# Performance work log

Measured on AMD Instinct MI355X. Metric: run time of the kernel, lower is better.

## Reference

```python
import jax, jax.numpy as jnp
import numpy as np

NH = 16

def sinusoidal_pos(pos, nh=NH):
    # pos: [B, L] -> P: [B, L, nh], interleaved sin/cos with integer multiples of pi
    freqs = jnp.arange(1, nh // 2 + 1, dtype=pos.dtype) * jnp.pi  # [nh/2]
    ang = pos[..., None] * freqs                                   # [B, L, nh/2]
    # interleave: even channels sin, odd channels cos
    P = jnp.stack([jnp.sin(ang), jnp.cos(ang)], axis=-1)           # [B, L, nh/2, 2]
    return P.reshape(*pos.shape, nh)


def setup_inputs() -> dict:
    key = jax.random.key(0)
    k1, k2, k3, k4, k5, k6 = jax.random.split(key, 6)
    B, L, nx, nh = 2048, 1024, 8, NH
    return {
        "x": jax.random.normal(k1, (B, L, nx), dtype=jnp.float32),
        "pos": jax.random.uniform(k2, (B, L), dtype=jnp.float32),
        "W_q": jax.random.normal(k3, (nh, nx), dtype=jnp.float32) * 0.1,
        "W_k": jax.random.normal(k4, (nh, nx), dtype=jnp.float32) * 0.1,
        "W_v": jax.random.normal(k5, (nh, nx), dtype=jnp.float32) * 0.1,
        "W_o": jax.random.normal(k6, (nh, nh), dtype=jnp.float32) * 0.1,
    }


def reference(x, pos, W_q, W_k, W_v, W_o):
    # x: [B, L, nx]; pos: [B, L]; Linear weights are [out, in] (torch convention)
    q = jnp.einsum("blx,hx->blh", x, W_q)
    k = jnp.einsum("blx,hx->blh", x, W_k)
    v = jnp.einsum("blx,hx->blh", x, W_v)
    P = sinusoidal_pos(pos, W_q.shape[0])
    q = q + P
    k = k + P
    L = q.shape[1]
    # channel-wise attention: score over feature dim, [B, nh, nh]
    score = jnp.einsum("bld,ble->bde", q, k) / jnp.sqrt(jnp.asarray(L, q.dtype))
    attn = jax.nn.softmax(score, axis=-1)
    out = jnp.einsum("bde,ble->bdl", attn, v)   # [B, nh, L]
    out = jnp.einsum("bdl,hd->blh", out, W_o)   # transpose then W_o: [B, L, nh]
    return out
```

## Files before the change

kernel.cpp:

```cpp
#include <hip/hip_runtime.h>
#include <cstdint>
#include <cstddef>

#define LSEQ 1024
#define NH   16
#define NX   8

__device__ __forceinline__ uint32_t f2bf(float f) {
    uint32_t u = __float_as_uint(f);
    u += 0x7fffu + ((u >> 16) & 1u);
    return u >> 16;
}
__device__ __forceinline__ float bflo(uint32_t w) { return __uint_as_float(w << 16); }
__device__ __forceinline__ float bfhi(uint32_t w) { return __uint_as_float(w & 0xffff0000u); }

__global__ __launch_bounds__(256, 1)
void attn_fused_kernel(const float* __restrict__ x, const float* __restrict__ pos,
                       const float* __restrict__ Wq, const float* __restrict__ Wk,
                       const float* __restrict__ Wv, const float* __restrict__ Wo,
                       float* __restrict__ out) {
    __shared__ __align__(16) char smem_raw[65536];
    uint16_t* q_lds = (uint16_t*)smem_raw;
    uint16_t* k_lds = (uint16_t*)(smem_raw + 32768);
    float* scorebuf = (float*)smem_raw;
    float* attn_s   = (float*)(smem_raw + 4096);
    float* M_s      = (float*)(smem_raw + 5120);
    float* weff_s   = (float*)(smem_raw + 6144);

    const int tid = threadIdx.x;
    const int b   = blockIdx.x;
    const float* xb = x   + (size_t)b * LSEQ * NX;
    const float* pb = pos + (size_t)b * LSEQ;

    {
        const int dg   = tid >> 6;
        const int lidx = tid & 63;
        float wq[4][8], wk[4][8];
        #pragma unroll
        for (int r = 0; r < 4; ++r) {
            const float4 a0 = *(const float4*)(Wq + (4 * dg + r) * 8);
            const float4 a1 = *(const float4*)(Wq + (4 * dg + r) * 8 + 4);
            const float4 b0 = *(const float4*)(Wk + (4 * dg + r) * 8);
            const float4 b1 = *(const float4*)(Wk + (4 * dg + r) * 8 + 4);
            wq[r][0]=a0.x; wq[r][1]=a0.y; wq[r][2]=a0.z; wq[r][3]=a0.w;
            wq[r][4]=a1.x; wq[r][5]=a1.y; wq[r][6]=a1.z; wq[r][7]=a1.w;
            wk[r][0]=b0.x; wk[r][1]=b0.y; wk[r][2]=b0.z; wk[r][3]=b0.w;
            wk[r][4]=b1.x; wk[r][5]=b1.y; wk[r][6]=b1.z; wk[r][7]=b1.w;
        }
        const float f0 = (float)(2 * dg + 1);
        const float f1 = (float)(2 * dg + 2);
        for (int p = 0; p < 16; ++p) {
            const int l = p * 64 + lidx;
            const float4 xa = *(const float4*)(xb + (size_t)l * 8);
            const float4 xc = *(const float4*)(xb + (size_t)l * 8 + 4);
            const float pv = pb[l];
            float pe[4];
            pe[0] = sinpif(pv * f0); pe[1] = cospif(pv * f0);
            pe[2] = sinpif(pv * f1); pe[3] = cospif(pv * f1);
            float qv[4], kv[4];
            #pragma unroll
            for (int r = 0; r < 4; ++r) {
                qv[r] = xa.x*wq[r][0] + xa.y*wq[r][1] + xa.z*wq[r][2] + xa.w*wq[r][3]
                      + xc.x*wq[r][4] + xc.y*wq[r][5] + xc.z*wq[r][6] + xc.w*wq[r][7] + pe[r];
                kv[r] = xa.x*wk[r][0] + xa.y*wk[r][1] + xa.z*wk[r][2] + xa.w*wk[r][3]
                      + xc.x*wk[r][4] + xc.y*wk[r][5] + xc.z*wk[r][6] + xc.w*wk[r][7] + pe[r];
            }
            uint2 qp, kp;
            qp.x = f2bf(qv[0]) | (f2bf(qv[1]) << 16);
            qp.y = f2bf(qv[2]) | (f2bf(qv[3]) << 16);
            kp.x = f2bf(kv[0]) | (f2bf(kv[1]) << 16);
            kp.y = f2bf(kv[2]) | (f2bf(kv[3]) << 16);
            *(uint2*)(q_lds + (size_t)l * 16 + 4 * dg) = qp;
            *(uint2*)(k_lds + (size_t)l * 16 + 4 * dg) = kp;
        }
    }
    __syncthreads();

    {
        const int lg = tid >> 4;
        const int dt = (tid >> 2) & 3;
        const int et = tid & 3;
        float acc[4][4];
        #pragma unroll
        for (int i = 0; i < 4; ++i)
            #pragma unroll
            for (int j = 0; j < 4; ++j) acc[i][j] = 0.f;

        const uint16_t* qp = q_lds + lg * 16 + dt * 4;
        const uint16_t* kp = k_lds + lg * 16 + et * 4;
        #pragma unroll 4
        for (int i = 0; i < 64; ++i) {
            const uint2 qw = *(const uint2*)(qp + i * 256);
            const uint2 kw = *(const uint2*)(kp + i * 256);
            const float q0 = bflo(qw.x), q1 = bfhi(qw.x), q2 = bflo(qw.y), q3 = bfhi(qw.y);
            const float k0 = bflo(kw.x), k1 = bfhi(kw.x), k2 = bflo(kw.y), k3 = bfhi(kw.y);
            acc[0][0] += q0*k0; acc[0][1] += q0*k1; acc[0][2] += q0*k2; acc[0][3] += q0*k3;
            acc[1][0] += q1*k0; acc[1][1] += q1*k1; acc[1][2] += q1*k2; acc[1][3] += q1*k3;
            acc[2][0] += q2*k0; acc[2][1] += q2*k1; acc[2][2] += q2*k2; acc[2][3] += q2*k3;
            acc[3][0] += q3*k0; acc[3][1] += q3*k1; acc[3][2] += q3*k2; acc[3][3] += q3*k3;
        }
        #pragma unroll
        for (int di = 0; di < 4; ++di)
            #pragma unroll
            for (int ei = 0; ei < 4; ++ei) {
                acc[di][ei] += __shfl_xor(acc[di][ei], 16);
                acc[di][ei] += __shfl_xor(acc[di][ei], 32);
            }
        __syncthreads();
        const int lane = tid & 63;
        const int w    = tid >> 6;
        if (lane < 16) {
            #pragma unroll
            for (int di = 0; di < 4; ++di)
                #pragma unroll
                for (int ei = 0; ei < 4; ++ei)
                    scorebuf[w * 256 + (dt * 4 + di) * 16 + (et * 4 + ei)] = acc[di][ei];
        }
    }
    __syncthreads();

    {
        const int e = tid & 15;
        float s = scorebuf[tid] + scorebuf[256 + tid] + scorebuf[512 + tid] + scorebuf[768 + tid];
        s *= 0.03125f;
        float mx = s;
        #pragma unroll
        for (int m = 1; m < 16; m <<= 1) mx = fmaxf(mx, __shfl_xor(mx, m));
        const float ex = __expf(s - mx);
        float sum = ex;
        #pragma unroll
        for (int m = 1; m < 16; m <<= 1) sum += __shfl_xor(sum, m);
        attn_s[tid] = ex / sum;
        __syncthreads();

        const int h = tid >> 4;
        float acc = 0.f;
        #pragma unroll
        for (int d = 0; d < 16; ++d) acc += Wo[h * 16 + d] * attn_s[d * 16 + e];
        M_s[h * 16 + e] = acc;
        __syncthreads();

        if (tid < 128) {
            const int hh = tid >> 3, xc = tid & 7;
            float wv = 0.f;
            #pragma unroll
            for (int ee = 0; ee < 16; ++ee) wv += M_s[hh * 16 + ee] * Wv[ee * 8 + xc];
            weff_s[hh * 8 + xc] = wv;
        }
    }
    __syncthreads();

    {
        float xr[4][8];
        #pragma unroll
        for (int r = 0; r < 4; ++r) {
            const int l = tid + 256 * r;
            const float4 a = *(const float4*)(xb + (size_t)l * 8);
            const float4 c = *(const float4*)(xb + (size_t)l * 8 + 4);
            xr[r][0]=a.x; xr[r][1]=a.y; xr[r][2]=a.z; xr[r][3]=a.w;
            xr[r][4]=c.x; xr[r][5]=c.y; xr[r][6]=c.z; xr[r][7]=c.w;
        }
        float o[4][16];
        #pragma unroll
        for (int h = 0; h < 16; ++h) {
            const float4 wA = *(const float4*)(weff_s + h * 8);
            const float4 wB = *(const float4*)(weff_s + h * 8 + 4);
            #pragma unroll
            for (int r = 0; r < 4; ++r) {
                o[r][h] = xr[r][0]*wA.x + xr[r][1]*wA.y + xr[r][2]*wA.z + xr[r][3]*wA.w
                        + xr[r][4]*wB.x + xr[r][5]*wB.y + xr[r][6]*wB.z + xr[r][7]*wB.w;
            }
        }
        #pragma unroll
        for (int r = 0; r < 4; ++r) {
            const size_t base = ((size_t)b * LSEQ + tid + 256 * r) * NH;
            #pragma unroll
            for (int g = 0; g < 4; ++g) {
                *(float4*)(out + base + g * 4) =
                    make_float4(o[r][g*4+0], o[r][g*4+1], o[r][g*4+2], o[r][g*4+3]);
            }
        }
    }
}

extern "C" void kernel_launch(void* const* d_in, const int* in_sizes, int n_in,
                              void* d_out, int out_size, void* d_ws, size_t ws_size,
                              hipStream_t stream) {
    const float* x   = (const float*)d_in[0];
    const float* pos = (const float*)d_in[1];
    const float* Wq  = (const float*)d_in[2];
    const float* Wk  = (const float*)d_in[3];
    const float* Wv  = (const float*)d_in[4];
    const float* Wo  = (const float*)d_in[5];
    float* out = (float*)d_out;
    const int B = in_sizes[1] / LSEQ;
    attn_fused_kernel<<<B, 256, 0, stream>>>(x, pos, Wq, Wk, Wv, Wo, out);
}
```

Measured before the change: 97.68 us.

## Split fused attention into chunked score-partial kernel and output kernel

```diff
diff --git a/kernel.cpp b/kernel.cpp
--- a/kernel.cpp
+++ b/kernel.cpp
@@ -2,9 +2,12 @@
 #include <cstdint>
 #include <cstddef>
 
-#define LSEQ 1024
-#define NH   16
-#define NX   8
+#define LSEQ   1024
+#define NH     16
+#define NX     8
+#define CHUNKS 4
+#define ROWS   256
+#define STR    20
 
 __device__ __forceinline__ uint32_t f2bf(float f) {
     uint32_t u = __float_as_uint(f);
@@ -13,6 +16,187 @@
 }
 __device__ __forceinline__ float bflo(uint32_t w) { return __uint_as_float(w << 16); }
 __device__ __forceinline__ float bfhi(uint32_t w) { return __uint_as_float(w & 0xffff0000u); }
+
+__global__ __launch_bounds__(256, 4)
+void score_partial_kernel(const float* __restrict__ x, const float* __restrict__ pos,
+                          const float* __restrict__ Wq, const float* __restrict__ Wk,
+                          float* __restrict__ g_part) {
+    __shared__ __align__(16) uint16_t q_lds[ROWS * STR];
+    __shared__ __align__(16) uint16_t k_lds[ROWS * STR];
+    __shared__ float scorebuf[4 * 256];
+
+    const int tid = threadIdx.x;
+    const int bid = blockIdx.x;
+    const int b   = bid >> 2;
+    const int c   = bid & 3;
+    const float* xb = x   + ((size_t)b * LSEQ + c * ROWS) * NX;
+    const float* pb = pos + (size_t)b * LSEQ + c * ROWS;
+
+    {
+        const int dg   = tid >> 6;
+        const int lidx = tid & 63;
+        float wq[4][8], wk[4][8];
+        #pragma unroll
+        for (int r = 0; r < 4; ++r) {
+            const float4 a0 = *(const float4*)(Wq + (4 * dg + r) * 8);
+            const float4 a1 = *(const float4*)(Wq + (4 * dg + r) * 8 + 4);
+            const float4 b0 = *(const float4*)(Wk + (4 * dg + r) * 8);
+            const float4 b1 = *(const float4*)(Wk + (4 * dg + r) * 8 + 4);
+            wq[r][0]=a0.x; wq[r][1]=a0.y; wq[r][2]=a0.z; wq[r][3]=a0.w;
+            wq[r][4]=a1.x; wq[r][5]=a1.y; wq[r][6]=a1.z; wq[r][7]=a1.w;
+            wk[r][0]=b0.x; wk[r][1]=b0.y; wk[r][2]=b0.z; wk[r][3]=b0.w;
+            wk[r][4]=b1.x; wk[r][5]=b1.y; wk[r][6]=b1.z; wk[r][7]=b1.w;
+        }
+        const float f0 = (float)(2 * dg + 1);
+        const float f1 = (float)(2 * dg + 2);
+        #pragma unroll
+        for (int p = 0; p < ROWS / 64; ++p) {
+            const int l = p * 64 + lidx;
+            const float4 xa = *(const float4*)(xb + (size_t)l * 8);
+            const float4 xc = *(const float4*)(xb + (size_t)l * 8 + 4);
+            const float pv = pb[l];
+            float pe[4];
+            pe[0] = sinpif(pv * f0); pe[1] = cospif(pv * f0);
+            pe[2] = sinpif(pv * f1); pe[3] = cospif(pv * f1);
+            float qv[4], kv[4];
+            #pragma unroll
+            for (int r = 0; r < 4; ++r) {
+                qv[r] = xa.x*wq[r][0] + xa.y*wq[r][1] + xa.z*wq[r][2] + xa.w*wq[r][3]
+                      + xc.x*wq[r][4] + xc.y*wq[r][5] + xc.z*wq[r][6] + xc.w*wq[r][7] + pe[r];
+                kv[r] = xa.x*wk[r][0] + xa.y*wk[r][1] + xa.z*wk[r][2] + xa.w*wk[r][3]
+                      + xc.x*wk[r][4] + xc.y*wk[r][5] + xc.z*wk[r][6] + xc.w*wk[r][7] + pe[r];
+            }
+            uint2 qp, kp;
+            qp.x = f2bf(qv[0]) | (f2bf(qv[1]) << 16);
+            qp.y = f2bf(qv[2]) | (f2bf(qv[3]) << 16);
+            kp.x = f2bf(kv[0]) | (f2bf(kv[1]) << 16);
+            kp.y = f2bf(kv[2]) | (f2bf(kv[3]) << 16);
+            *(uint2*)(q_lds + (size_t)l * STR + 4 * dg) = qp;
+            *(uint2*)(k_lds + (size_t)l * STR + 4 * dg) = kp;
+        }
+    }
+    __syncthreads();
+
+    {
+        const int lg = tid >> 4;
+        const int dt = (tid >> 2) & 3;
+        const int et = tid & 3;
+        float acc[4][4];
+        #pragma unroll
+        for (int i = 0; i < 4; ++i)
+            #pragma unroll
+            for (int j = 0; j < 4; ++j) acc[i][j] = 0.f;
+
+        const uint16_t* qp = q_lds + lg * STR + dt * 4;
+        const uint16_t* kp = k_lds + lg * STR + et * 4;
+        #pragma unroll 4
+        for (int i = 0; i < ROWS / 16; ++i) {
+            const uint2 qw = *(const uint2*)(qp + i * 16 * STR);
+            const uint2 kw = *(const uint2*)(kp + i * 16 * STR);
+            const float q0 = bflo(qw.x), q1 = bfhi(qw.x), q2 = bflo(qw.y), q3 = bfhi(qw.y);
+            const float k0 = bflo(kw.x), k1 = bfhi(kw.x), k2 = bflo(kw.y), k3 = bfhi(kw.y);
+            acc[0][0] += q0*k0; acc[0][1] += q0*k1; acc[0][2] += q0*k2; acc[0][3] += q0*k3;
+            acc[1][0] += q1*k0; acc[1][1] += q1*k1; acc[1][2] += q1*k2; acc[1][3] += q1*k3;
+            acc[2][0] += q2*k0; acc[2][1] += q2*k1; acc[2][2] += q2*k2; acc[2][3] += q2*k3;
+            acc[3][0] += q3*k0; acc[3][1] += q3*k1; acc[3][2] += q3*k2; acc[3][3] += q3*k3;
+        }
+        #pragma unroll
+        for (int di = 0; di < 4; ++di)
+            #pragma unroll
+            for (int ei = 0; ei < 4; ++ei) {
+                acc[di][ei] += __shfl_xor(acc[di][ei], 16);
+                acc[di][ei] += __shfl_xor(acc[di][ei], 32);
+            }
+        const int lane = tid & 63;
+        const int w    = tid >> 6;
+        if (lane < 16) {
+            #pragma unroll
+            for (int di = 0; di < 4; ++di)
+                #pragma unroll
+                for (int ei = 0; ei < 4; ++ei)
+                    scorebuf[w * 256 + (dt * 4 + di) * 16 + (et * 4 + ei)] = acc[di][ei];
+        }
+    }
+    __syncthreads();
+    g_part[(size_t)bid * 256 + tid] =
+        scorebuf[tid] + scorebuf[256 + tid] + scorebuf[512 + tid] + scorebuf[768 + tid];
+}
+
+__global__ __launch_bounds__(256, 4)
+void out_kernel(const float* __restrict__ x, const float* __restrict__ Wv,
+                const float* __restrict__ Wo, const float* __restrict__ g_part,
+                float* __restrict__ out) {
+    __shared__ float attn_s[256];
+    __shared__ float M_s[256];
+    __shared__ float weff_s[128];
+
+    const int tid = threadIdx.x;
+    const int b   = blockIdx.x;
+    const float* xb = x + (size_t)b * LSEQ * NX;
+
+    {
+        const float* gp = g_part + (size_t)(b * CHUNKS) * 256 + tid;
+        float s = gp[0] + gp[256] + gp[512] + gp[768];
+        s *= 0.03125f;
+        float mx = s;
+        #pragma unroll
+        for (int m = 1; m < 16; m <<= 1) mx = fmaxf(mx, __shfl_xor(mx, m));
+        const float ex = __expf(s - mx);
+        float sum = ex;
+        #pragma unroll
+        for (int m = 1; m < 16; m <<= 1) sum += __shfl_xor(sum, m);
+        attn_s[tid] = ex / sum;
+    }
+    __syncthreads();
+    {
+        const int h = tid >> 4, e = tid & 15;
+        float acc = 0.f;
+        #pragma unroll
+        for (int d = 0; d < 16; ++d) acc += Wo[h * 16 + d] * attn_s[d * 16 + e];
+        M_s[h * 16 + e] = acc;
+    }
+    __syncthreads();
+    if (tid < 128) {
+        const int hh = tid >> 3, xc = tid & 7;
+        float wv = 0.f;
+        #pragma unroll
+        for (int ee = 0; ee < 16; ++ee) wv += M_s[hh * 16 + ee] * Wv[ee * 8 + xc];
+        weff_s[hh * 8 + xc] = wv;
+    }
+    __syncthreads();
+
+    {
+        float xr[4][8];
+        #pragma unroll
+        for (int r = 0; r < 4; ++r) {
+            const int l = tid + 256 * r;
+            const float4 a = *(const float4*)(xb + (size_t)l * 8);
+            const float4 c = *(const float4*)(xb + (size_t)l * 8 + 4);
+            xr[r][0]=a.x; xr[r][1]=a.y; xr[r][2]=a.z; xr[r][3]=a.w;
+            xr[r][4]=c.x; xr[r][5]=c.y; xr[r][6]=c.z; xr[r][7]=c.w;
+        }
+        float o[4][16];
+        #pragma unroll
+        for (int h = 0; h < 16; ++h) {
+            const float4 wA = *(const float4*)(weff_s + h * 8);
+            const float4 wB = *(const float4*)(weff_s + h * 8 + 4);
+            #pragma unroll
+            for (int r = 0; r < 4; ++r) {
+                o[r][h] = xr[r][0]*wA.x + xr[r][1]*wA.y + xr[r][2]*wA.z + xr[r][3]*wA.w
+                        + xr[r][4]*wB.x + xr[r][5]*wB.y + xr[r][6]*wB.z + xr[r][7]*wB.w;
+            }
+        }
+        #pragma unroll
+        for (int r = 0; r < 4; ++r) {
+            const size_t base = ((size_t)b * LSEQ + tid + 256 * r) * NH;
+            #pragma unroll
+            for (int g = 0; g < 4; ++g) {
+                *(float4*)(out + base + g * 4) =
+                    make_float4(o[r][g*4+0], o[r][g*4+1], o[r][g*4+2], o[r][g*4+3]);
+            }
+        }
+    }
+}
 
 __global__ __launch_bounds__(256, 1)
 void attn_fused_kernel(const float* __restrict__ x, const float* __restrict__ pos,
@@ -75,7 +259,6 @@
         }
     }
     __syncthreads();
-
     {
         const int lg = tid >> 4;
         const int dt = (tid >> 2) & 3;
@@ -85,7 +268,6 @@
         for (int i = 0; i < 4; ++i)
             #pragma unroll
             for (int j = 0; j < 4; ++j) acc[i][j] = 0.f;
-
         const uint16_t* qp = q_lds + lg * 16 + dt * 4;
         const uint16_t* kp = k_lds + lg * 16 + et * 4;
         #pragma unroll 4
@@ -118,9 +300,7 @@
         }
     }
     __syncthreads();
-
-    {
-        const int e = tid & 15;
+    {
         float s = scorebuf[tid] + scorebuf[256 + tid] + scorebuf[512 + tid] + scorebuf[768 + tid];
         s *= 0.03125f;
         float mx = s;
@@ -132,14 +312,12 @@
         for (int m = 1; m < 16; m <<= 1) sum += __shfl_xor(sum, m);
         attn_s[tid] = ex / sum;
         __syncthreads();
-
-        const int h = tid >> 4;
+        const int h = tid >> 4, e = tid & 15;
         float acc = 0.f;
         #pragma unroll
         for (int d = 0; d < 16; ++d) acc += Wo[h * 16 + d] * attn_s[d * 16 + e];
         M_s[h * 16 + e] = acc;
         __syncthreads();
-
         if (tid < 128) {
             const int hh = tid >> 3, xc = tid & 7;
             float wv = 0.f;
@@ -149,7 +327,6 @@
         }
     }
     __syncthreads();
-
     {
         float xr[4][8];
         #pragma unroll
@@ -194,5 +371,13 @@
     const float* Wo  = (const float*)d_in[5];
     float* out = (float*)d_out;
     const int B = in_sizes[1] / LSEQ;
-    attn_fused_kernel<<<B, 256, 0, stream>>>(x, pos, Wq, Wk, Wv, Wo, out);
-}
+
+    const size_t ws_needed = (size_t)B * CHUNKS * 256 * sizeof(float);
+    if (ws_size >= ws_needed) {
+        float* g_part = (float*)d_ws;
+        score_partial_kernel<<<B * CHUNKS, 256, 0, stream>>>(x, pos, Wq, Wk, g_part);
+        out_kernel<<<B, 256, 0, stream>>>(x, Wv, Wo, g_part, out);
+    } else {
+        attn_fused_kernel<<<B, 256, 0, stream>>>(x, pos, Wq, Wk, Wv, Wo, out);
+    }
+}
```

After: 159.1 us. 1.63x slower.

## Use 512-thread blocks with XOR-swizzled LDS layout for Q/K

Applied to the files above, without the earlier changes.

```diff
diff --git a/kernel.cpp b/kernel.cpp
--- a/kernel.cpp
+++ b/kernel.cpp
@@ -14,18 +14,18 @@
 __device__ __forceinline__ float bflo(uint32_t w) { return __uint_as_float(w << 16); }
 __device__ __forceinline__ float bfhi(uint32_t w) { return __uint_as_float(w & 0xffff0000u); }
 
-__global__ __launch_bounds__(256, 1)
-void attn_fused_kernel(const float* __restrict__ x, const float* __restrict__ pos,
-                       const float* __restrict__ Wq, const float* __restrict__ Wk,
-                       const float* __restrict__ Wv, const float* __restrict__ Wo,
-                       float* __restrict__ out) {
+__global__ __launch_bounds__(512, 4)
+void attn_fused512(const float* __restrict__ x, const float* __restrict__ pos,
+                   const float* __restrict__ Wq, const float* __restrict__ Wk,
+                   const float* __restrict__ Wv, const float* __restrict__ Wo,
+                   float* __restrict__ out) {
     __shared__ __align__(16) char smem_raw[65536];
     uint16_t* q_lds = (uint16_t*)smem_raw;
     uint16_t* k_lds = (uint16_t*)(smem_raw + 32768);
     float* scorebuf = (float*)smem_raw;
-    float* attn_s   = (float*)(smem_raw + 4096);
-    float* M_s      = (float*)(smem_raw + 5120);
-    float* weff_s   = (float*)(smem_raw + 6144);
+    float* attn_s   = (float*)(smem_raw + 8192);
+    float* M_s      = (float*)(smem_raw + 9216);
+    float* weff_s   = (float*)(smem_raw + 10240);
 
     const int tid = threadIdx.x;
     const int b   = blockIdx.x;
@@ -33,8 +33,8 @@
     const float* pb = pos + (size_t)b * LSEQ;
 
     {
-        const int dg   = tid >> 6;
-        const int lidx = tid & 63;
+        const int dg   = tid >> 7;
+        const int lidx = tid & 127;
         float wq[4][8], wk[4][8];
         #pragma unroll
         for (int r = 0; r < 4; ++r) {
@@ -49,8 +49,9 @@
         }
         const float f0 = (float)(2 * dg + 1);
         const float f1 = (float)(2 * dg + 2);
-        for (int p = 0; p < 16; ++p) {
-            const int l = p * 64 + lidx;
+        #pragma unroll
+        for (int p = 0; p < 8; ++p) {
+            const int l = p * 128 + lidx;
             const float4 xa = *(const float4*)(xb + (size_t)l * 8);
             const float4 xc = *(const float4*)(xb + (size_t)l * 8 + 4);
             const float pv = pb[l];
@@ -70,28 +71,30 @@
             qp.y = f2bf(qv[2]) | (f2bf(qv[3]) << 16);
             kp.x = f2bf(kv[0]) | (f2bf(kv[1]) << 16);
             kp.y = f2bf(kv[2]) | (f2bf(kv[3]) << 16);
-            *(uint2*)(q_lds + (size_t)l * 16 + 4 * dg) = qp;
-            *(uint2*)(k_lds + (size_t)l * 16 + 4 * dg) = kp;
-        }
-    }
-    __syncthreads();
-
+            const int sw = ((l >> 2) & 3) ^ dg;
+            *(uint2*)(q_lds + (size_t)l * 16 + sw * 4) = qp;
+            *(uint2*)(k_lds + (size_t)l * 16 + sw * 4) = kp;
+        }
+    }
+    __syncthreads();
+
+    float acc[4][4];
     {
         const int lg = tid >> 4;
         const int dt = (tid >> 2) & 3;
         const int et = tid & 3;
-        float acc[4][4];
         #pragma unroll
         for (int i = 0; i < 4; ++i)
             #pragma unroll
             for (int j = 0; j < 4; ++j) acc[i][j] = 0.f;
 
-        const uint16_t* qp = q_lds + lg * 16 + dt * 4;
-        const uint16_t* kp = k_lds + lg * 16 + et * 4;
+        const int s = (lg >> 2) & 3;
+        const uint16_t* qp = q_lds + lg * 16 + (dt ^ s) * 4;
+        const uint16_t* kp = k_lds + lg * 16 + (et ^ s) * 4;
         #pragma unroll 4
-        for (int i = 0; i < 64; ++i) {
-            const uint2 qw = *(const uint2*)(qp + i * 256);
-            const uint2 kw = *(const uint2*)(kp + i * 256);
+        for (int i = 0; i < 32; ++i) {
+            const uint2 qw = *(const uint2*)(qp + i * 512);
+            const uint2 kw = *(const uint2*)(kp + i * 512);
             const float q0 = bflo(qw.x), q1 = bfhi(qw.x), q2 = bflo(qw.y), q3 = bfhi(qw.y);
             const float k0 = bflo(kw.x), k1 = bfhi(kw.x), k2 = bflo(kw.y), k3 = bfhi(kw.y);
             acc[0][0] += q0*k0; acc[0][1] += q0*k1; acc[0][2] += q0*k2; acc[0][3] += q0*k3;
@@ -119,9 +122,10 @@
     }
     __syncthreads();
 
-    {
-        const int e = tid & 15;
-        float s = scorebuf[tid] + scorebuf[256 + tid] + scorebuf[512 + tid] + scorebuf[768 + tid];
+    if (tid < 256) {
+        float s = 0.f;
+        #pragma unroll
+        for (int w = 0; w < 8; ++w) s += scorebuf[w * 256 + tid];
         s *= 0.03125f;
         float mx = s;
         #pragma unroll
@@ -131,49 +135,49 @@
         #pragma unroll
         for (int m = 1; m < 16; m <<= 1) sum += __shfl_xor(sum, m);
         attn_s[tid] = ex / sum;
-        __syncthreads();
-
-        const int h = tid >> 4;
-        float acc = 0.f;
-        #pragma unroll
-        for (int d = 0; d < 16; ++d) acc += Wo[h * 16 + d] * attn_s[d * 16 + e];
-        M_s[h * 16 + e] = acc;
-        __syncthreads();
-
-        if (tid < 128) {
-            const int hh = tid >> 3, xc = tid & 7;
-            float wv = 0.f;
-            #pragma unroll
-            for (int ee = 0; ee < 16; ++ee) wv += M_s[hh * 16 + ee] * Wv[ee * 8 + xc];
-            weff_s[hh * 8 + xc] = wv;
-        }
+    }
+    __syncthreads();
+    if (tid < 256) {
+        const int h = tid >> 4, e = tid & 15;
+        float acc2 = 0.f;
+        #pragma unroll
+        for (int d = 0; d < 16; ++d) acc2 += Wo[h * 16 + d] * attn_s[d * 16 + e];
+        M_s[h * 16 + e] = acc2;
+    }
+    __syncthreads();
+    if (tid < 128) {
+        const int hh = tid >> 3, xc = tid & 7;
+        float wv = 0.f;
+        #pragma unroll
+        for (int ee = 0; ee < 16; ++ee) wv += M_s[hh * 16 + ee] * Wv[ee * 8 + xc];
+        weff_s[hh * 8 + xc] = wv;
     }
     __syncthreads();
 
     {
-        float xr[4][8];
-        #pragma unroll
-        for (int r = 0; r < 4; ++r) {
-            const int l = tid + 256 * r;
+        float xr[2][8];
+        #pragma unroll
+        for (int r = 0; r < 2; ++r) {
+            const int l = tid + 512 * r;
             const float4 a = *(const float4*)(xb + (size_t)l * 8);
             const float4 c = *(const float4*)(xb + (size_t)l * 8 + 4);
             xr[r][0]=a.x; xr[r][1]=a.y; xr[r][2]=a.z; xr[r][3]=a.w;
             xr[r][4]=c.x; xr[r][5]=c.y; xr[r][6]=c.z; xr[r][7]=c.w;
         }
-        float o[4][16];
+        float o[2][16];
         #pragma unroll
         for (int h = 0; h < 16; ++h) {
             const float4 wA = *(const float4*)(weff_s + h * 8);
             const float4 wB = *(const float4*)(weff_s + h * 8 + 4);
             #pragma unroll
-            for (int r = 0; r < 4; ++r) {
+            for (int r = 0; r < 2; ++r) {
                 o[r][h] = xr[r][0]*wA.x + xr[r][1]*wA.y + xr[r][2]*wA.z + xr[r][3]*wA.w
                         + xr[r][4]*wB.x + xr[r][5]*wB.y + xr[r][6]*wB.z + xr[r][7]*wB.w;
             }
         }
         #pragma unroll
-        for (int r = 0; r < 4; ++r) {
-            const size_t base = ((size_t)b * LSEQ + tid + 256 * r) * NH;
+        for (int r = 0; r < 2; ++r) {
+            const size_t base = ((size_t)b * LSEQ + tid + 512 * r) * NH;
             #pragma unroll
             for (int g = 0; g < 4; ++g) {
                 *(float4*)(out + base + g * 4) =
@@ -194,5 +198,5 @@
     const float* Wo  = (const float*)d_in[5];
     float* out = (float*)d_out;
     const int B = in_sizes[1] / LSEQ;
-    attn_fused_kernel<<<B, 256, 0, stream>>>(x, pos, Wq, Wk, Wv, Wo, out);
+    attn_fused512<<<B, 512, 0, stream>>>(x, pos, Wq, Wk, Wv, Wo, out);
 }
```

Result: slower. 164.6 us (+68.5%).
